# Kernel tuning notes

Hardware: AMD Instinct MI355X
Metric: run time of the kernel (lower is better)

The kernel has to match this reference:

```python
import jax, jax.numpy as jnp
import numpy as np

_BN_EPS = 1e-5
_BN_SCALE = 1.0 / np.sqrt(1.0 + _BN_EPS)  # eval-mode BN with running_mean=0, running_var=1


def _bn(x, g, b):
    # eval-mode BatchNorm1d over channel dim (last axis here)
    return x * (g * _BN_SCALE) + b


def _sa_layer(src_xyz, dst_xyz, cur_i, idx, empty, p_w, p_g, p_b, m_w, m_g, m_b):
    # src_xyz: (N,3), dst_xyz: (M,3), cur_i: (N,D), idx: (M,S) int, empty: (M,) bool
    idx = idx.astype(jnp.int32)
    sp = src_xyz[idx]                       # (M,S,3) neighbor gather
    dp = dst_xyz[:, None, :]                # (M,1,3)
    feat6 = jnp.concatenate([sp - dp, jnp.broadcast_to(dp, sp.shape)], axis=-1)  # (M,S,6)
    off = jax.nn.silu(_bn(jnp.einsum('msc,dc->msd', feat6, p_w), p_g, p_b))      # (M,S,D)
    x = off + cur_i[idx]                    # (M,S,D)
    x = jnp.where(empty[:, None, None], 0.0, x)
    h = jax.nn.relu(_bn(jnp.einsum('msd,hd->msh', x, m_w), m_g, m_b))            # (M,S,H)
    return jnp.max(h, axis=1)               # (M,H) max-pool over neighbors


def reference(src_xyz, src_feats, dst_xyz, idx0, idx1, empty0, empty1,
              fc0_w, fc0_b, p0_w, p0_g, p0_b, m0_w, m0_g, m0_b,
              fc1_w, fc1_b, p1_w, p1_g, p1_b, m1_w, m1_g, m1_b,
              out_w, out_g, out_b):
    cur0 = src_feats @ fc0_w.T + fc0_b      # (N,64) fc_i of layer 0
    cur1 = src_feats @ fc1_w.T + fc1_b      # (N,64) fc_i of layer 1
    f0 = _sa_layer(src_xyz, dst_xyz, cur0, idx0, empty0, p0_w, p0_g, p0_b, m0_w, m0_g, m0_b)
    f1 = _sa_layer(src_xyz, dst_xyz, cur1, idx1, empty1, p1_w, p1_g, p1_b, m1_w, m1_g, m1_b)
    feats = jnp.concatenate([f0, f1], axis=1)                                    # (M,256)
    out = jax.nn.relu(_bn(feats @ out_w.T, out_g, out_b))                        # out_conv (1x1 conv)
    return out                               # (M,256)


def setup_inputs() -> dict:
    key = jax.random.key(0)
    ks = jax.random.split(key, 24)
    N, M, Cin, D, H, S0, S1 = 65536, 16384, 64, 64, 128, 16, 32
    inp = {
        'src_xyz': jax.random.normal(ks[0], (N, 3), jnp.float32) * 20.0,
        'src_feats': jax.random.normal(ks[1], (N, Cin), jnp.float32),
        'dst_xyz': jax.random.normal(ks[2], (M, 3), jnp.float32) * 20.0,
        'idx0': jax.random.randint(ks[3], (M, S0), 0, N, jnp.int32),
        'idx1': jax.random.randint(ks[4], (M, S1), 0, N, jnp.int32),
        'empty0': jax.random.bernoulli(ks[5], 0.05, (M,)),
        'empty1': jax.random.bernoulli(ks[6], 0.05, (M,)),
        'fc0_w': jax.random.normal(ks[7], (D, Cin), jnp.float32) / np.sqrt(Cin),
        'fc0_b': jnp.zeros((D,), jnp.float32),
        'p0_w': jax.random.normal(ks[8], (D, 6), jnp.float32) / np.sqrt(6.0),
        'p0_g': jnp.ones((D,), jnp.float32),
        'p0_b': jnp.zeros((D,), jnp.float32),
        'm0_w': jax.random.normal(ks[9], (H, D), jnp.float32) / np.sqrt(D),
        'm0_g': jnp.ones((H,), jnp.float32),
        'm0_b': jnp.zeros((H,), jnp.float32),
        'fc1_w': jax.random.normal(ks[10], (D, Cin), jnp.float32) / np.sqrt(Cin),
        'fc1_b': jnp.zeros((D,), jnp.float32),
        'p1_w': jax.random.normal(ks[11], (D, 6), jnp.float32) / np.sqrt(6.0),
        'p1_g': jnp.ones((D,), jnp.float32),
        'p1_b': jnp.zeros((D,), jnp.float32),
        'm1_w': jax.random.normal(ks[12], (H, D), jnp.float32) / np.sqrt(D),
        'm1_g': jnp.ones((H,), jnp.float32),
        'm1_b': jnp.zeros((H,), jnp.float32),
        'out_w': jax.random.normal(ks[13], (256, 2 * H), jnp.float32) / np.sqrt(2.0 * H),
        'out_g': jnp.ones((256,), jnp.float32),
        'out_b': jnp.zeros((256,), jnp.float32),
    }
    return inp
```

## Files before the change

### kernel.cpp

```cpp
#include <hip/hip_runtime.h>

typedef unsigned short ushort_t;
typedef unsigned int uint_t;
typedef __attribute__((ext_vector_type(8))) short v8s;
typedef __attribute__((ext_vector_type(4))) float v4f;

#define BN_SCALE 0.9999950000374997f

__device__ __forceinline__ float bf2f(ushort_t u) {
    union { uint_t i; float f; } v;
    v.i = ((uint_t)u) << 16;
    return v.f;
}
__device__ __forceinline__ ushort_t f2bf(float f) {
    union { uint_t i; float f; } v;
    v.f = f;
    uint_t b = v.i;
    b += 0x7fffu + ((b >> 16) & 1u);
    return (ushort_t)(b >> 16);
}

__device__ __forceinline__ v8s cvt8(const float* __restrict__ p) {
    v8s f;
    #pragma unroll
    for (int j = 0; j < 8; ++j) f[j] = (short)f2bf(p[j]);
    return f;
}

__global__ __launch_bounds__(256) void convw_kernel(
    const float* __restrict__ w, ushort_t* __restrict__ wb)
{
    const int i = (blockIdx.x * 256 + threadIdx.x) * 4;
    const v4f v = *(const v4f*)(w + i);
    ushort_t r0 = f2bf(v[0]), r1 = f2bf(v[1]), r2 = f2bf(v[2]), r3 = f2bf(v[3]);
    uint_t lo = (uint_t)r0 | ((uint_t)r1 << 16);
    uint_t hi = (uint_t)r2 | ((uint_t)r3 << 16);
    *(uint2*)(wb + i) = make_uint2(lo, hi);
}

__global__ __launch_bounds__(256) void cur_kernel(
    const float* __restrict__ src_feats,
    const float* __restrict__ fc0_w, const float* __restrict__ fc0_b,
    const float* __restrict__ fc1_w, const float* __restrict__ fc1_b,
    ushort_t* __restrict__ cur0, ushort_t* __restrict__ cur1)
{
    const int tid  = threadIdx.x;
    const int lane = tid & 63;
    const int wid  = tid >> 6;
    const int col  = lane & 15;
    const int quad = lane >> 4;
    const int row0 = blockIdx.x * 64 + wid * 16;

    v8s afrag[2];
    #pragma unroll
    for (int kf = 0; kf < 2; ++kf)
        afrag[kf] = cvt8(src_feats + (size_t)(row0 + col) * 64 + kf * 32 + quad * 8);

    v4f acc[8];
    v8s bfrag[8][2];
    #pragma unroll
    for (int ct = 0; ct < 8; ++ct) {
        const int d = (ct & 3) * 16 + col;
        const float* w = (ct < 4 ? fc0_w : fc1_w) + d * 64;
        const float  b = (ct < 4 ? fc0_b : fc1_b)[d];
        acc[ct] = (v4f){b, b, b, b};
        #pragma unroll
        for (int kf = 0; kf < 2; ++kf)
            bfrag[ct][kf] = cvt8(w + kf * 32 + quad * 8);
    }

    #pragma unroll
    for (int kf = 0; kf < 2; ++kf)
        #pragma unroll
        for (int ct = 0; ct < 8; ++ct)
            acc[ct] = __builtin_amdgcn_mfma_f32_16x16x32_bf16(
                afrag[kf], bfrag[ct][kf], acc[ct], 0, 0, 0);

    #pragma unroll
    for (int ct = 0; ct < 8; ++ct) {
        ushort_t* dst = (ct < 4) ? cur0 : cur1;
        const int d = (ct & 3) * 16 + col;
        #pragma unroll
        for (int r = 0; r < 4; ++r) {
            const int n = row0 + quad * 4 + r;
            dst[(size_t)n * 64 + d] = f2bf(acc[ct][r]);
        }
    }
}

template <int S>
__global__ __launch_bounds__(256, 4) void sa_kernel(
    const float* __restrict__ src_xyz,
    const float* __restrict__ dst_xyz,
    const int*   __restrict__ idx,
    const int*   __restrict__ empty,
    const float* __restrict__ p_w,
    const float* __restrict__ p_g,
    const float* __restrict__ p_b,
    const float* __restrict__ m_w,
    const float* __restrict__ m_g,
    const float* __restrict__ m_b,
    const ushort_t* __restrict__ cur,
    ushort_t*    __restrict__ f01,
    int layer_off)
{
    constexpr int MB = 256 / S;
    constexpr int XP = 72;
    constexpr int T  = S / 4;
    __shared__ ushort_t xlds[MB * S * XP];
    __shared__ v4f      flds[256];

    const int tid  = threadIdx.x;
    const int lane = tid & 63;
    const int wid  = tid >> 6;
    const int m0   = blockIdx.x * MB;

    {
        const int mi = tid / S;
        const int m  = m0 + mi;
        const int i  = idx[(size_t)m * S + (tid & (S - 1))];
        const float dx = dst_xyz[m * 3 + 0];
        const float dy = dst_xyz[m * 3 + 1];
        const float dz = dst_xyz[m * 3 + 2];
        v4f r;
        r[0] = src_xyz[i * 3 + 0] - dx;
        r[1] = src_xyz[i * 3 + 1] - dy;
        r[2] = src_xyz[i * 3 + 2] - dz;
        r[3] = __int_as_float(i);
        flds[tid] = r;
    }

    const int d = lane;
    const float pg = p_g[d] * BN_SCALE;
    const float pb = p_b[d];
    const float pwg0 = p_w[d * 6 + 0] * pg;
    const float pwg1 = p_w[d * 6 + 1] * pg;
    const float pwg2 = p_w[d * 6 + 2] * pg;
    const float pd0  = p_w[d * 6 + 3] * pg;
    const float pd1  = p_w[d * 6 + 4] * pg;
    const float pd2  = p_w[d * 6 + 5] * pg;

    const int col  = lane & 15;
    const int quad = lane >> 4;
    v8s bfrag[2][2];
    float mgv[2], mbv[2];
    #pragma unroll
    for (int c = 0; c < 2; ++c) {
        const int h = (wid * 2 + c) * 16 + col;
        #pragma unroll
        for (int kf = 0; kf < 2; ++kf)
            bfrag[c][kf] = cvt8(m_w + h * 64 + kf * 32 + quad * 8);
        mgv[c] = m_g[h] * BN_SCALE;
        mbv[c] = m_b[h];
    }

    __syncthreads();

    const ushort_t* cur_d = cur + d;
    const int tbase = wid * T;
    #pragma unroll
    for (int mi = 0; mi < MB; ++mi) {
        const int m = m0 + mi;
        const float dx = dst_xyz[m * 3 + 0];
        const float dy = dst_xyz[m * 3 + 1];
        const float dz = dst_xyz[m * 3 + 2];
        const float vbase = fmaf(pd0, dx, fmaf(pd1, dy, fmaf(pd2, dz, pb)));
        const int em = empty[m];

        v4f rr[T];
        #pragma unroll
        for (int tt = 0; tt < T; ++tt)
            rr[tt] = flds[mi * S + tbase + tt];

        float cf[T];
        #pragma unroll
        for (int tt = 0; tt < T; ++tt)
            cf[tt] = bf2f(cur_d[(size_t)__float_as_int(rr[tt][3]) * 64]);

        #pragma unroll
        for (int tt = 0; tt < T; ++tt) {
            const float v = fmaf(pwg0, rr[tt][0],
                            fmaf(pwg1, rr[tt][1],
                            fmaf(pwg2, rr[tt][2], vbase)));
            const float e  = __expf(-v);
            const float rc = __builtin_amdgcn_rcpf(1.0f + e);
            float x = fmaf(v, rc, cf[tt]);
            x = em ? 0.0f : x;
            xlds[(mi * S + tbase + tt) * XP + d] = f2bf(x);
        }
    }
    __syncthreads();

    #pragma unroll
    for (int mi = 0; mi < MB; ++mi) {
        const int m = m0 + mi;
        v4f acc[S / 16][2];
        #pragma unroll
        for (int rt = 0; rt < S / 16; ++rt)
            #pragma unroll
            for (int c = 0; c < 2; ++c)
                acc[rt][c] = (v4f)0.0f;

        #pragma unroll
        for (int rt = 0; rt < S / 16; ++rt) {
            #pragma unroll
            for (int kf = 0; kf < 2; ++kf) {
                const v8s afrag = *(const v8s*)(
                    xlds + ((mi * S + rt * 16 + col)) * XP + kf * 32 + quad * 8);
                acc[rt][0] = __builtin_amdgcn_mfma_f32_16x16x32_bf16(
                    afrag, bfrag[0][kf], acc[rt][0], 0, 0, 0);
                acc[rt][1] = __builtin_amdgcn_mfma_f32_16x16x32_bf16(
                    afrag, bfrag[1][kf], acc[rt][1], 0, 0, 0);
            }
        }

        float vmax0 = 0.0f, vmax1 = 0.0f;
        #pragma unroll
        for (int c = 0; c < 2; ++c) {
            float vm = 0.0f;
            #pragma unroll
            for (int rt = 0; rt < S / 16; ++rt)
                #pragma unroll
                for (int r = 0; r < 4; ++r) {
                    const float y = fmaf(acc[rt][c][r], mgv[c], mbv[c]);
                    vm = fmaxf(vm, y);
                }
            vm = fmaxf(vm, __shfl_xor(vm, 16));
            vm = fmaxf(vm, __shfl_xor(vm, 32));
            if (c == 0) vmax0 = vm; else vmax1 = vm;
        }
        if (lane < 32) {
            const int c = lane >> 4;
            const float val = (c == 0) ? vmax0 : vmax1;
            f01[m * 256 + layer_off + (wid * 2 + c) * 16 + (lane & 15)] = f2bf(val);
        }
    }
}

__global__ __launch_bounds__(256) void out_kernel(
    const ushort_t* __restrict__ f01,
    const ushort_t* __restrict__ out_wb,
    const float*    __restrict__ out_g,
    const float*    __restrict__ out_b,
    float*          __restrict__ out)
{
    const int tid  = threadIdx.x;
    const int lane = tid & 63;
    const int wid  = tid >> 6;
    const int col  = lane & 15;
    const int quad = lane >> 4;
    const int m0   = blockIdx.x * 16;

    v8s afrag[8];
    #pragma unroll
    for (int kf = 0; kf < 8; ++kf)
        afrag[kf] = *(const v8s*)(f01 + (size_t)(m0 + col) * 256 + kf * 32 + quad * 8);

    v4f acc[4];
    #pragma unroll
    for (int c = 0; c < 4; ++c) acc[c] = (v4f)0.0f;

    #pragma unroll
    for (int kf = 0; kf < 8; ++kf) {
        #pragma unroll
        for (int c = 0; c < 4; ++c) {
            const int n = (wid * 4 + c) * 16 + col;
            const v8s b = *(const v8s*)(out_wb + (size_t)n * 256 + kf * 32 + quad * 8);
            acc[c] = __builtin_amdgcn_mfma_f32_16x16x32_bf16(afrag[kf], b, acc[c], 0, 0, 0);
        }
    }

    #pragma unroll
    for (int c = 0; c < 4; ++c) {
        const int n  = (wid * 4 + c) * 16 + col;
        const float og = out_g[n] * BN_SCALE;
        const float ob = out_b[n];
        #pragma unroll
        for (int r = 0; r < 4; ++r) {
            float y = fmaf(acc[c][r], og, ob);
            y = fmaxf(y, 0.0f);
            out[(size_t)(m0 + quad * 4 + r) * 256 + n] = y;
        }
    }
}

extern "C" void kernel_launch(void* const* d_in, const int* in_sizes, int n_in,
                              void* d_out, int out_size, void* d_ws, size_t ws_size,
                              hipStream_t stream)
{
    const float* src_xyz   = (const float*)d_in[0];
    const float* src_feats = (const float*)d_in[1];
    const float* dst_xyz   = (const float*)d_in[2];
    const int*   idx0      = (const int*)d_in[3];
    const int*   idx1      = (const int*)d_in[4];
    const int*   empty0    = (const int*)d_in[5];
    const int*   empty1    = (const int*)d_in[6];
    const float* fc0_w     = (const float*)d_in[7];
    const float* fc0_b     = (const float*)d_in[8];
    const float* p0_w      = (const float*)d_in[9];
    const float* p0_g      = (const float*)d_in[10];
    const float* p0_b      = (const float*)d_in[11];
    const float* m0_w      = (const float*)d_in[12];
    const float* m0_g      = (const float*)d_in[13];
    const float* m0_b      = (const float*)d_in[14];
    const float* fc1_w     = (const float*)d_in[15];
    const float* fc1_b     = (const float*)d_in[16];
    const float* p1_w      = (const float*)d_in[17];
    const float* p1_g      = (const float*)d_in[18];
    const float* p1_b      = (const float*)d_in[19];
    const float* m1_w      = (const float*)d_in[20];
    const float* m1_g      = (const float*)d_in[21];
    const float* m1_b      = (const float*)d_in[22];
    const float* out_w     = (const float*)d_in[23];
    const float* out_g     = (const float*)d_in[24];
    const float* out_b     = (const float*)d_in[25];

    const int N = in_sizes[0] / 3;
    const int M = in_sizes[2] / 3;

    ushort_t* cur0   = (ushort_t*)d_ws;
    ushort_t* cur1   = cur0 + (size_t)N * 64;
    ushort_t* f01    = cur1 + (size_t)N * 64;
    ushort_t* out_wb = f01 + (size_t)M * 256;

    convw_kernel<<<64, 256, 0, stream>>>(out_w, out_wb);
    cur_kernel<<<N / 64, 256, 0, stream>>>(src_feats, fc0_w, fc0_b, fc1_w, fc1_b,
                                           cur0, cur1);
    sa_kernel<16><<<M / 16, 256, 0, stream>>>(src_xyz, dst_xyz, idx0, empty0,
                                              p0_w, p0_g, p0_b, m0_w, m0_g, m0_b,
                                              cur0, f01, 0);
    sa_kernel<32><<<M / 8, 256, 0, stream>>>(src_xyz, dst_xyz, idx1, empty1,
                                             p1_w, p1_g, p1_b, m1_w, m1_g, m1_b,
                                             cur1, f01, 128);
    out_kernel<<<M / 16, 256, 0, stream>>>(f01, out_wb, out_g, out_b,
                                           (float*)d_out);
}
```

Before: 210.0 us.

## Fuse both SA layers into one launch with smaller blocks

Both set-abstraction layers now run in a single kernel launch, with the block index picking the layer; the S=32 blocks are scheduled first. Each block now handles 128 neighbor pairs instead of 256, which halves the shared-memory footprint and raises the launch bound from 4 to 6 blocks per CU for better occupancy and fewer tail effects. The m_w fragment loads move after the gather phase to shorten register live ranges. In exchange there are twice as many blocks and more redundant per-block weight loads, and half the threads sit idle during the initial xyz gather.

```diff
diff --git a/kernel.cpp b/kernel.cpp
--- a/kernel.cpp
+++ b/kernel.cpp
@@ -89,7 +89,8 @@
 }
 
 template <int S>
-__global__ __launch_bounds__(256, 4) void sa_kernel(
+__device__ __forceinline__ void sa_body(
+    const int bid,
     const float* __restrict__ src_xyz,
     const float* __restrict__ dst_xyz,
     const int*   __restrict__ idx,
@@ -102,20 +103,21 @@
     const float* __restrict__ m_b,
     const ushort_t* __restrict__ cur,
     ushort_t*    __restrict__ f01,
-    int layer_off)
-{
-    constexpr int MB = 256 / S;
+    const int layer_off,
+    ushort_t* xlds,
+    v4f*      flds)
+{
+    constexpr int PAIRS = 128;
+    constexpr int MB = PAIRS / S;
     constexpr int XP = 72;
     constexpr int T  = S / 4;
-    __shared__ ushort_t xlds[MB * S * XP];
-    __shared__ v4f      flds[256];
 
     const int tid  = threadIdx.x;
     const int lane = tid & 63;
     const int wid  = tid >> 6;
-    const int m0   = blockIdx.x * MB;
-
-    {
+    const int m0   = bid * MB;
+
+    if (tid < PAIRS) {
         const int mi = tid / S;
         const int m  = m0 + mi;
         const int i  = idx[(size_t)m * S + (tid & (S - 1))];
@@ -140,20 +142,6 @@
     const float pd1  = p_w[d * 6 + 4] * pg;
     const float pd2  = p_w[d * 6 + 5] * pg;
 
-    const int col  = lane & 15;
-    const int quad = lane >> 4;
-    v8s bfrag[2][2];
-    float mgv[2], mbv[2];
-    #pragma unroll
-    for (int c = 0; c < 2; ++c) {
-        const int h = (wid * 2 + c) * 16 + col;
-        #pragma unroll
-        for (int kf = 0; kf < 2; ++kf)
-            bfrag[c][kf] = cvt8(m_w + h * 64 + kf * 32 + quad * 8);
-        mgv[c] = m_g[h] * BN_SCALE;
-        mbv[c] = m_b[h];
-    }
-
     __syncthreads();
 
     const ushort_t* cur_d = cur + d;
@@ -172,23 +160,37 @@
         for (int tt = 0; tt < T; ++tt)
             rr[tt] = flds[mi * S + tbase + tt];
 
-        float cf[T];
+        ushort_t cfu[T];
         #pragma unroll
         for (int tt = 0; tt < T; ++tt)
-            cf[tt] = bf2f(cur_d[(size_t)__float_as_int(rr[tt][3]) * 64]);
+            cfu[tt] = cur_d[(size_t)__float_as_int(rr[tt][3]) * 64];
 
         #pragma unroll
         for (int tt = 0; tt < T; ++tt) {
             const float v = fmaf(pwg0, rr[tt][0],
                             fmaf(pwg1, rr[tt][1],
                             fmaf(pwg2, rr[tt][2], vbase)));
-            const float e  = __expf(-v);
-            const float rc = __builtin_amdgcn_rcpf(1.0f + e);
-            float x = fmaf(v, rc, cf[tt]);
+            const float rc = __builtin_amdgcn_rcpf(1.0f + __expf(-v));
+            float x = fmaf(v, rc, bf2f(cfu[tt]));
             x = em ? 0.0f : x;
             xlds[(mi * S + tbase + tt) * XP + d] = f2bf(x);
         }
     }
+
+    const int col  = lane & 15;
+    const int quad = lane >> 4;
+    v8s bfrag[2][2];
+    float mgv[2], mbv[2];
+    #pragma unroll
+    for (int c = 0; c < 2; ++c) {
+        const int h = (wid * 2 + c) * 16 + col;
+        #pragma unroll
+        for (int kf = 0; kf < 2; ++kf)
+            bfrag[c][kf] = cvt8(m_w + h * 64 + kf * 32 + quad * 8);
+        mgv[c] = m_g[h] * BN_SCALE;
+        mbv[c] = m_b[h];
+    }
+
     __syncthreads();
 
     #pragma unroll
@@ -235,6 +237,30 @@
             f01[m * 256 + layer_off + (wid * 2 + c) * 16 + (lane & 15)] = f2bf(val);
         }
     }
+}
+
+__global__ __launch_bounds__(256, 6) void sa_fused_kernel(
+    const float* __restrict__ src_xyz, const float* __restrict__ dst_xyz,
+    const int* __restrict__ idx0, const int* __restrict__ empty0,
+    const float* __restrict__ p0_w, const float* __restrict__ p0_g, const float* __restrict__ p0_b,
+    const float* __restrict__ m0_w, const float* __restrict__ m0_g, const float* __restrict__ m0_b,
+    const ushort_t* __restrict__ cur0,
+    const int* __restrict__ idx1, const int* __restrict__ empty1,
+    const float* __restrict__ p1_w, const float* __restrict__ p1_g, const float* __restrict__ p1_b,
+    const float* __restrict__ m1_w, const float* __restrict__ m1_g, const float* __restrict__ m1_b,
+    const ushort_t* __restrict__ cur1,
+    ushort_t* __restrict__ f01, const int G32)
+{
+    __shared__ ushort_t xlds[128 * 72];
+    __shared__ v4f      flds[128];
+
+    const int b = blockIdx.x;
+    if (b < G32)
+        sa_body<32>(b, src_xyz, dst_xyz, idx1, empty1, p1_w, p1_g, p1_b,
+                    m1_w, m1_g, m1_b, cur1, f01, 128, xlds, flds);
+    else
+        sa_body<16>(b - G32, src_xyz, dst_xyz, idx0, empty0, p0_w, p0_g, p0_b,
+                    m0_w, m0_g, m0_b, cur0, f01, 0, xlds, flds);
 }
 
 __global__ __launch_bounds__(256) void out_kernel(
@@ -323,15 +349,17 @@
     ushort_t* f01    = cur1 + (size_t)N * 64;
     ushort_t* out_wb = f01 + (size_t)M * 256;
 
+    const int G32 = M / 4;
+    const int G16 = M / 8;
+
     convw_kernel<<<64, 256, 0, stream>>>(out_w, out_wb);
     cur_kernel<<<N / 64, 256, 0, stream>>>(src_feats, fc0_w, fc0_b, fc1_w, fc1_b,
                                            cur0, cur1);
-    sa_kernel<16><<<M / 16, 256, 0, stream>>>(src_xyz, dst_xyz, idx0, empty0,
-                                              p0_w, p0_g, p0_b, m0_w, m0_g, m0_b,
-                                              cur0, f01, 0);
-    sa_kernel<32><<<M / 8, 256, 0, stream>>>(src_xyz, dst_xyz, idx1, empty1,
-                                             p1_w, p1_g, p1_b, m1_w, m1_g, m1_b,
-                                             cur1, f01, 128);
+    sa_fused_kernel<<<G32 + G16, 256, 0, stream>>>(
+        src_xyz, dst_xyz,
+        idx0, empty0, p0_w, p0_g, p0_b, m0_w, m0_g, m0_b, cur0,
+        idx1, empty1, p1_w, p1_g, p1_b, m1_w, m1_g, m1_b, cur1,
+        f01, G32);
     out_kernel<<<M / 16, 256, 0, stream>>>(f01, out_wb, out_g, out_b,
                                            (float*)d_out);
 }
```

Result: faster. 204.7 us (-2.5%).
